# Optimization experiments

Hardware: AMD Instinct MI355X
Metric: run time of the kernel (lower is better)

Reference implementation:

```python
import jax, jax.numpy as jnp
import numpy as np

N, K = 50000, 16
D_IN, D_EDGE, D_HID, D_OUT = 128, 64, 32, 128


def setup_inputs() -> dict:
    key = jax.random.key(0)
    ks = jax.random.split(key, 10)
    s = lambda fan_in: 1.0 / np.sqrt(fan_in)
    return {
        'x': jax.random.normal(ks[0], (N, D_IN), jnp.float32),
        'neibs': jax.random.normal(ks[1], (N * K, D_IN), jnp.float32),
        'edge_emb': jax.random.normal(ks[2], (N * K, D_EDGE), jnp.float32),
        'mask': (jax.random.uniform(ks[3], (N, K)) < 0.3).astype(jnp.float32),
        # att: Linear(D_IN->H) -> tanh -> Linear(H->H); stored as [in,out]
        'W_att1_a': jax.random.uniform(ks[4], (D_IN, D_HID), jnp.float32, -s(D_IN), s(D_IN)),
        'W_att1_b': jax.random.uniform(ks[5], (D_HID, D_HID), jnp.float32, -s(D_HID), s(D_HID)),
        # att2 operates on concat(neibs, edge_emb)
        'W_att2_a': jax.random.uniform(ks[6], (D_IN + D_EDGE, D_HID), jnp.float32, -s(D_IN + D_EDGE), s(D_IN + D_EDGE)),
        'W_att2_b': jax.random.uniform(ks[7], (D_HID, D_HID), jnp.float32, -s(D_HID), s(D_HID)),
        'W_fc_x': jax.random.uniform(ks[8], (D_IN, D_OUT), jnp.float32, -s(D_IN), s(D_IN)),
        'W_fc_neib': jax.random.uniform(ks[9], (D_IN + D_EDGE, D_OUT), jnp.float32, -s(D_IN + D_EDGE), s(D_IN + D_EDGE)),
    }


def reference(x, neibs, edge_emb, mask, W_att1_a, W_att1_b, W_att2_a, W_att2_b, W_fc_x, W_fc_neib):
    n, k = mask.shape
    ne = jnp.concatenate([neibs, edge_emb], axis=1)            # [N*K, D_IN+D_EDGE]
    neib_att = jnp.tanh(ne @ W_att2_a) @ W_att2_b               # [N*K, H]
    x_att = jnp.tanh(x @ W_att1_a) @ W_att1_b                   # [N, H]
    ws = jnp.einsum('nkh,nh->nk', neib_att.reshape(n, k, -1), x_att)
    ws = jax.nn.softmax(ws + (-9999999.0) * mask, axis=1)       # masked softmax over neighbors
    agg_neib = jnp.einsum('nkd,nk->nd', ne.reshape(n, k, -1), ws)
    out = jnp.concatenate([x @ W_fc_x, agg_neib @ W_fc_neib], axis=1)  # concat_node=True
    return jax.nn.elu(out)  # dropout p=0.0 (eval), batchnorm=False
```

## Files before the change

kernel.cpp:

```cpp
#include <hip/hip_runtime.h>
#include <math.h>


typedef _Float16 half_t;
typedef __attribute__((ext_vector_type(4))) _Float16 half4_t;
typedef __attribute__((ext_vector_type(8))) _Float16 half8_t;
typedef __attribute__((ext_vector_type(4))) float f32x4;

#define NN   50000
#define GK   16
#define DIN  128
#define DED  64
#define DNE  192

#define WS_M    0
#define WS_W1A  4096
#define WS_W2A  12288
#define WS_WFX  24576
#define WS_WFN  57344

__device__ __forceinline__ void swz(const float* __restrict__ W, int ncol, int S,
                                    half_t* __restrict__ dst, int tid, int nth) {
  int T = ncol >> 4;
  int total = T * S * 512;
  for (int i = tid; i < total; i += nth) {
    int j = i & 7;
    int l = (i >> 3) & 63;
    int rest = i >> 9;
    int s = rest % S;
    int t = rest / S;
    int k = 32 * s + (l >> 4) * 8 + j;
    int n = 16 * t + (l & 15);
    dst[i] = (half_t)W[k * ncol + n];
  }
}

__global__ void setup_kernel(const float* __restrict__ W1a, const float* __restrict__ W1b,
                             const float* __restrict__ W2a, const float* __restrict__ W2b,
                             const float* __restrict__ Wfx, const float* __restrict__ Wfn,
                             unsigned char* __restrict__ ws) {
  int tid = blockIdx.x * blockDim.x + threadIdx.x;
  int nth = gridDim.x * blockDim.x;
  float* Mm = (float*)(ws + WS_M);
  for (int i = tid; i < 1024; i += nth) {
    int a = i >> 5, h = i & 31;
    float acc = 0.f;
    for (int h2 = 0; h2 < 32; ++h2)
      acc = fmaf(W1b[a * 32 + h2], W2b[h * 32 + h2], acc);
    Mm[i] = acc;
  }
  swz(W1a, 32, 4, (half_t*)(ws + WS_W1A), tid, nth);
  swz(W2a, 32, 6, (half_t*)(ws + WS_W2A), tid, nth);
  swz(Wfx, 128, 4, (half_t*)(ws + WS_WFX), tid, nth);
  swz(Wfn, 128, 6, (half_t*)(ws + WS_WFN), tid, nth);
}

__device__ __forceinline__ half8_t cvt8(float4 a, float4 b) {
  half8_t r;
  r[0] = (half_t)a.x; r[1] = (half_t)a.y; r[2] = (half_t)a.z; r[3] = (half_t)a.w;
  r[4] = (half_t)b.x; r[5] = (half_t)b.y; r[6] = (half_t)b.z; r[7] = (half_t)b.w;
  return r;
}

__device__ __forceinline__ float elu(float v) { return v > 0.f ? v : expm1f(v); }

__global__ __launch_bounds__(256, 4)
void pre_kernel(const float* __restrict__ x, const unsigned char* __restrict__ ws,
                float* __restrict__ out) {
  __shared__ float t1L[64][33];
  const int tid = threadIdx.x;
  const int wave = tid >> 6, lane = tid & 63;
  const int l15 = lane & 15, q = lane >> 4;
  const int nb0 = blockIdx.x * 64;
  const int n0 = nb0 + wave * 16;
  const float* Mm = (const float*)(ws + WS_M);
  const half_t* w1a = (const half_t*)(ws + WS_W1A);
  const half_t* wfx = (const half_t*)(ws + WS_WFX);

  int row = n0 + l15; if (row >= NN) row = NN - 1;
  const float* xrow = x + (size_t)row * DIN;
  half8_t Ax[4];
  f32x4 t0acc = {0.f, 0.f, 0.f, 0.f}, t1acc = {0.f, 0.f, 0.f, 0.f};
#pragma unroll
  for (int s = 0; s < 4; ++s) {
    float4 a0 = *(const float4*)(xrow + 32 * s + 8 * q);
    float4 a1 = *(const float4*)(xrow + 32 * s + 8 * q + 4);
    Ax[s] = cvt8(a0, a1);
    half8_t B0 = *(const half8_t*)(w1a + ((size_t)(0 * 4 + s) * 64 + lane) * 8);
    half8_t B1 = *(const half8_t*)(w1a + ((size_t)(1 * 4 + s) * 64 + lane) * 8);
    t0acc = __builtin_amdgcn_mfma_f32_16x16x32_f16(Ax[s], B0, t0acc, 0, 0, 0);
    t1acc = __builtin_amdgcn_mfma_f32_16x16x32_f16(Ax[s], B1, t1acc, 0, 0, 0);
  }
#pragma unroll
  for (int r = 0; r < 4; ++r) {
    t1L[wave * 16 + 4 * q + r][l15]      = tanhf(t0acc[r]);
    t1L[wave * 16 + 4 * q + r][16 + l15] = tanhf(t1acc[r]);
  }
  __syncthreads();

#pragma unroll
  for (int i = 0; i < 8; ++i) {
    int idx = i * 256 + tid;
    int g = idx >> 5, h = idx & 31;
    float acc = 0.f;
#pragma unroll
    for (int a = 0; a < 32; ++a)
      acc = fmaf(t1L[g][a], Mm[a * 32 + h], acc);
    int n = nb0 + g;
    if (n < NN) out[(size_t)n * 256 + 128 + h] = acc;
  }

#pragma unroll
  for (int t = 0; t < 8; ++t) {
    f32x4 acc = {0.f, 0.f, 0.f, 0.f};
#pragma unroll
    for (int s = 0; s < 4; ++s) {
      half8_t B = *(const half8_t*)(wfx + ((size_t)(t * 4 + s) * 64 + lane) * 8);
      acc = __builtin_amdgcn_mfma_f32_16x16x32_f16(Ax[s], B, acc, 0, 0, 0);
    }
#pragma unroll
    for (int r = 0; r < 4; ++r) {
      int m = n0 + 4 * q + r;
      if (m < NN) out[(size_t)m * 256 + t * 16 + l15] = elu(acc[r]);
    }
  }
}

__global__ __launch_bounds__(512, 6)
void attn_kernel(const float* __restrict__ neibs, const float* __restrict__ edge,
                 const float* __restrict__ mask, const unsigned char* __restrict__ ws,
                 float* __restrict__ out) {
  __shared__ __align__(16) half_t aggL[16][200];
  const int tid = threadIdx.x;
  const int wave = tid >> 6, lane = tid & 63;
  const int l15 = lane & 15, q = lane >> 4;
  const int n = blockIdx.x * 8 + wave;
  const half_t* w2a = (const half_t*)(ws + WS_W2A);
  const half_t* wfn = (const half_t*)(ws + WS_WFN);

  for (int i = tid; i < 800; i += 512)
    ((unsigned int*)&aggL[8][0])[i] = 0u;

  f32x4 acc0 = {0.f, 0.f, 0.f, 0.f}, acc1 = {0.f, 0.f, 0.f, 0.f};
  const float* nbase = neibs + (size_t)n * (GK * DIN);
  const float* ebase = edge + (size_t)n * (GK * DED);
  const float* nrow = nbase + l15 * DIN;
  const float* erow = ebase + l15 * DED;
#pragma unroll
  for (int s = 0; s < 4; ++s) {
    float4 a0 = *(const float4*)(nrow + 32 * s + 8 * q);
    float4 a1 = *(const float4*)(nrow + 32 * s + 8 * q + 4);
    half8_t A = cvt8(a0, a1);
    half8_t B0 = *(const half8_t*)(w2a + ((size_t)(0 * 6 + s) * 64 + lane) * 8);
    half8_t B1 = *(const half8_t*)(w2a + ((size_t)(1 * 6 + s) * 64 + lane) * 8);
    acc0 = __builtin_amdgcn_mfma_f32_16x16x32_f16(A, B0, acc0, 0, 0, 0);
    acc1 = __builtin_amdgcn_mfma_f32_16x16x32_f16(A, B1, acc1, 0, 0, 0);
  }
#pragma unroll
  for (int s = 0; s < 2; ++s) {
    float4 a0 = *(const float4*)(erow + 32 * s + 8 * q);
    float4 a1 = *(const float4*)(erow + 32 * s + 8 * q + 4);
    half8_t A = cvt8(a0, a1);
    half8_t B0 = *(const half8_t*)(w2a + ((size_t)(0 * 6 + 4 + s) * 64 + lane) * 8);
    half8_t B1 = *(const half8_t*)(w2a + ((size_t)(1 * 6 + 4 + s) * 64 + lane) * 8);
    acc0 = __builtin_amdgcn_mfma_f32_16x16x32_f16(A, B0, acc0, 0, 0, 0);
    acc1 = __builtin_amdgcn_mfma_f32_16x16x32_f16(A, B1, acc1, 0, 0, 0);
  }

  const float u0 = out[(size_t)n * 256 + 128 + l15];
  const float u1 = out[(size_t)n * 256 + 144 + l15];

  float sv[4];
#pragma unroll
  for (int r = 0; r < 4; ++r)
    sv[r] = tanhf(acc0[r]) * u0 + tanhf(acc1[r]) * u1;
#pragma unroll
  for (int off = 1; off <= 8; off <<= 1)
#pragma unroll
    for (int r = 0; r < 4; ++r)
      sv[r] += __shfl_xor(sv[r], off);

  float e[4];
  float mx = -3.4e38f;
#pragma unroll
  for (int r = 0; r < 4; ++r) {
    sv[r] -= 9999999.0f * mask[(size_t)n * GK + 4 * q + r];
    mx = fmaxf(mx, sv[r]);
  }
  mx = fmaxf(mx, __shfl_xor(mx, 16));
  mx = fmaxf(mx, __shfl_xor(mx, 32));
  float sm = 0.f;
#pragma unroll
  for (int r = 0; r < 4; ++r) { e[r] = expf(sv[r] - mx); sm += e[r]; }
  sm += __shfl_xor(sm, 16);
  sm += __shfl_xor(sm, 32);
  const float rs = 1.0f / sm;
#pragma unroll
  for (int r = 0; r < 4; ++r) e[r] *= rs;

  float a0 = 0.f, a1 = 0.f, a2 = 0.f;
#pragma unroll
  for (int k = 0; k < GK; ++k) {
    float wv = __shfl(e[k & 3], (k & 12) << 2);
    a0 = fmaf(wv, nbase[k * DIN + lane], a0);
    a1 = fmaf(wv, nbase[k * DIN + 64 + lane], a1);
    a2 = fmaf(wv, ebase[k * DED + lane], a2);
  }
  aggL[wave][lane] = (half_t)a0;
  aggL[wave][64 + lane] = (half_t)a1;
  aggL[wave][128 + lane] = (half_t)a2;
  __syncthreads();

  f32x4 accn = {0.f, 0.f, 0.f, 0.f};
#pragma unroll
  for (int s = 0; s < 6; ++s) {
    half8_t A = *(const half8_t*)(&aggL[l15][32 * s + 8 * q]);
    half8_t B = *(const half8_t*)(wfn + ((size_t)(wave * 6 + s) * 64 + lane) * 8);
    accn = __builtin_amdgcn_mfma_f32_16x16x32_f16(A, B, accn, 0, 0, 0);
  }
  const size_t ob = (size_t)blockIdx.x * 8 * 256;
#pragma unroll
  for (int r = 0; r < 4; ++r) {
    int m = 4 * q + r;
    if (m < 8)
      out[ob + (size_t)m * 256 + 128 + wave * 16 + l15] = elu(accn[r]);
  }
}

extern "C" void kernel_launch(void* const* d_in, const int* in_sizes, int n_in,
                              void* d_out, int out_size, void* d_ws, size_t ws_size,
                              hipStream_t stream) {
  const float* x     = (const float*)d_in[0];
  const float* neibs = (const float*)d_in[1];
  const float* edge  = (const float*)d_in[2];
  const float* mask  = (const float*)d_in[3];
  const float* W1a   = (const float*)d_in[4];
  const float* W1b   = (const float*)d_in[5];
  const float* W2a   = (const float*)d_in[6];
  const float* W2b   = (const float*)d_in[7];
  const float* Wfx   = (const float*)d_in[8];
  const float* Wfn   = (const float*)d_in[9];
  float* out = (float*)d_out;
  unsigned char* ws = (unsigned char*)d_ws;

  hipLaunchKernelGGL(setup_kernel, dim3(64), dim3(256), 0, stream,
                     W1a, W1b, W2a, W2b, Wfx, Wfn, ws);
  hipLaunchKernelGGL(pre_kernel, dim3((NN + 63) / 64), dim3(256), 0, stream,
                     x, ws, out);
  hipLaunchKernelGGL(attn_kernel, dim3(NN / 8), dim3(512), 0, stream,
                     neibs, edge, mask, ws, out);
}
```

Baseline: 738.7 us.

## Fuse node-side projection kernel into attention kernel

Removes the separate pre_kernel and folds its work into attn_kernel. Each wave now computes the x-attention vector and one 16-column tile of the ELU(x@W_fc_x) output for its block's 8 nodes. The attention vector goes through a small per-wave LDS buffer instead of being written to the output buffer and read back. This drops one kernel launch and a global write/read round trip. In exchange, half of each x-side MFMA tile is wasted on duplicated rows, and the launch bound's occupancy hint falls from 6 to 4 blocks.

```diff
diff --git a/kernel.cpp b/kernel.cpp
--- a/kernel.cpp
+++ b/kernel.cpp
@@ -64,82 +64,75 @@
 
 __device__ __forceinline__ float elu(float v) { return v > 0.f ? v : expm1f(v); }
 
-__global__ __launch_bounds__(256, 4)
-void pre_kernel(const float* __restrict__ x, const unsigned char* __restrict__ ws,
-                float* __restrict__ out) {
-  __shared__ float t1L[64][33];
+__global__ __launch_bounds__(512, 4)
+void attn_kernel(const float* __restrict__ x, const float* __restrict__ neibs,
+                 const float* __restrict__ edge, const float* __restrict__ mask,
+                 const unsigned char* __restrict__ ws, float* __restrict__ out) {
+  __shared__ __align__(16) half_t aggL[16][200];
+  __shared__ float t1L[8][33];
   const int tid = threadIdx.x;
   const int wave = tid >> 6, lane = tid & 63;
   const int l15 = lane & 15, q = lane >> 4;
-  const int nb0 = blockIdx.x * 64;
-  const int n0 = nb0 + wave * 16;
+  const int n = blockIdx.x * 8 + wave;
   const float* Mm = (const float*)(ws + WS_M);
   const half_t* w1a = (const half_t*)(ws + WS_W1A);
+  const half_t* w2a = (const half_t*)(ws + WS_W2A);
   const half_t* wfx = (const half_t*)(ws + WS_WFX);
-
-  int row = n0 + l15; if (row >= NN) row = NN - 1;
-  const float* xrow = x + (size_t)row * DIN;
+  const half_t* wfn = (const half_t*)(ws + WS_WFN);
+
+  for (int i = tid; i < 800; i += 512)
+    ((unsigned int*)&aggL[8][0])[i] = 0u;
+
+  const float* xrow = x + (size_t)(blockIdx.x * 8 + (l15 & 7)) * DIN;
   half8_t Ax[4];
-  f32x4 t0acc = {0.f, 0.f, 0.f, 0.f}, t1acc = {0.f, 0.f, 0.f, 0.f};
 #pragma unroll
   for (int s = 0; s < 4; ++s) {
     float4 a0 = *(const float4*)(xrow + 32 * s + 8 * q);
     float4 a1 = *(const float4*)(xrow + 32 * s + 8 * q + 4);
     Ax[s] = cvt8(a0, a1);
-    half8_t B0 = *(const half8_t*)(w1a + ((size_t)(0 * 4 + s) * 64 + lane) * 8);
-    half8_t B1 = *(const half8_t*)(w1a + ((size_t)(1 * 4 + s) * 64 + lane) * 8);
-    t0acc = __builtin_amdgcn_mfma_f32_16x16x32_f16(Ax[s], B0, t0acc, 0, 0, 0);
-    t1acc = __builtin_amdgcn_mfma_f32_16x16x32_f16(Ax[s], B1, t1acc, 0, 0, 0);
-  }
-#pragma unroll
-  for (int r = 0; r < 4; ++r) {
-    t1L[wave * 16 + 4 * q + r][l15]      = tanhf(t0acc[r]);
-    t1L[wave * 16 + 4 * q + r][16 + l15] = tanhf(t1acc[r]);
-  }
-  __syncthreads();
-
-#pragma unroll
-  for (int i = 0; i < 8; ++i) {
-    int idx = i * 256 + tid;
-    int g = idx >> 5, h = idx & 31;
-    float acc = 0.f;
-#pragma unroll
-    for (int a = 0; a < 32; ++a)
-      acc = fmaf(t1L[g][a], Mm[a * 32 + h], acc);
-    int n = nb0 + g;
-    if (n < NN) out[(size_t)n * 256 + 128 + h] = acc;
-  }
-
-#pragma unroll
-  for (int t = 0; t < 8; ++t) {
-    f32x4 acc = {0.f, 0.f, 0.f, 0.f};
+  }
+
+  {
+    f32x4 t0 = {0.f, 0.f, 0.f, 0.f}, t1 = {0.f, 0.f, 0.f, 0.f};
 #pragma unroll
     for (int s = 0; s < 4; ++s) {
-      half8_t B = *(const half8_t*)(wfx + ((size_t)(t * 4 + s) * 64 + lane) * 8);
-      acc = __builtin_amdgcn_mfma_f32_16x16x32_f16(Ax[s], B, acc, 0, 0, 0);
+      half8_t B0 = *(const half8_t*)(w1a + ((size_t)(0 * 4 + s) * 64 + lane) * 8);
+      half8_t B1 = *(const half8_t*)(w1a + ((size_t)(1 * 4 + s) * 64 + lane) * 8);
+      t0 = __builtin_amdgcn_mfma_f32_16x16x32_f16(Ax[s], B0, t0, 0, 0, 0);
+      t1 = __builtin_amdgcn_mfma_f32_16x16x32_f16(Ax[s], B1, t1, 0, 0, 0);
     }
 #pragma unroll
     for (int r = 0; r < 4; ++r) {
-      int m = n0 + 4 * q + r;
-      if (m < NN) out[(size_t)m * 256 + t * 16 + l15] = elu(acc[r]);
-    }
-  }
-}
-
-__global__ __launch_bounds__(512, 6)
-void attn_kernel(const float* __restrict__ neibs, const float* __restrict__ edge,
-                 const float* __restrict__ mask, const unsigned char* __restrict__ ws,
-                 float* __restrict__ out) {
-  __shared__ __align__(16) half_t aggL[16][200];
-  const int tid = threadIdx.x;
-  const int wave = tid >> 6, lane = tid & 63;
-  const int l15 = lane & 15, q = lane >> 4;
-  const int n = blockIdx.x * 8 + wave;
-  const half_t* w2a = (const half_t*)(ws + WS_W2A);
-  const half_t* wfn = (const half_t*)(ws + WS_WFN);
-
-  for (int i = tid; i < 800; i += 512)
-    ((unsigned int*)&aggL[8][0])[i] = 0u;
+      if (4 * q + r == wave) {
+        t1L[wave][l15]      = tanhf(t0[r]);
+        t1L[wave][16 + l15] = tanhf(t1[r]);
+      }
+    }
+  }
+
+  float u0 = 0.f, u1 = 0.f;
+#pragma unroll
+  for (int a = 0; a < 32; ++a) {
+    float tv = t1L[wave][a];
+    u0 = fmaf(tv, Mm[a * 32 + l15], u0);
+    u1 = fmaf(tv, Mm[a * 32 + 16 + l15], u1);
+  }
+
+  {
+    f32x4 accx = {0.f, 0.f, 0.f, 0.f};
+#pragma unroll
+    for (int s = 0; s < 4; ++s) {
+      half8_t B = *(const half8_t*)(wfx + ((size_t)(wave * 4 + s) * 64 + lane) * 8);
+      accx = __builtin_amdgcn_mfma_f32_16x16x32_f16(Ax[s], B, accx, 0, 0, 0);
+    }
+    const size_t ob = (size_t)blockIdx.x * 8 * 256;
+#pragma unroll
+    for (int r = 0; r < 4; ++r) {
+      int m = 4 * q + r;
+      if (m < 8)
+        out[ob + (size_t)m * 256 + wave * 16 + l15] = elu(accx[r]);
+    }
+  }
 
   f32x4 acc0 = {0.f, 0.f, 0.f, 0.f}, acc1 = {0.f, 0.f, 0.f, 0.f};
   const float* nbase = neibs + (size_t)n * (GK * DIN);
@@ -166,9 +159,6 @@
     acc0 = __builtin_amdgcn_mfma_f32_16x16x32_f16(A, B0, acc0, 0, 0, 0);
     acc1 = __builtin_amdgcn_mfma_f32_16x16x32_f16(A, B1, acc1, 0, 0, 0);
   }
-
-  const float u0 = out[(size_t)n * 256 + 128 + l15];
-  const float u1 = out[(size_t)n * 256 + 144 + l15];
 
   float sv[4];
 #pragma unroll
@@ -245,8 +235,6 @@
 
   hipLaunchKernelGGL(setup_kernel, dim3(64), dim3(256), 0, stream,
                      W1a, W1b, W2a, W2b, Wfx, Wfn, ws);
-  hipLaunchKernelGGL(pre_kernel, dim3((NN + 63) / 64), dim3(256), 0, stream,
-                     x, ws, out);
   hipLaunchKernelGGL(attn_kernel, dim3(NN / 8), dim3(512), 0, stream,
-                     neibs, edge, mask, ws, out);
-}
+                     x, neibs, edge, mask, ws, out);
+}
```

After: 963.1 us. 1.3x slower.
